# Optimization experiments

Hardware: AMD Instinct MI355X
Metric: run time of the kernel (lower is better)

## Reference

```python
import jax, jax.numpy as jnp
import numpy as np

N = 10000      # nodes
E = 160000     # edges (before self loops)
G = 16         # graphs in batch
H = 4          # attention heads
F = 128        # hidden_dim (per-head out channels)
DIN = 64       # input_dim
NEG_SLOPE = 0.2


def setup_inputs() -> dict:
    key = jax.random.key(0)
    ks = jax.random.split(key, 20)
    x = jax.random.normal(ks[0], (N, DIN), jnp.float32)
    edge_index = jax.random.randint(ks[1], (2, E), 0, N, jnp.int32)
    batch = jnp.sort(jax.random.randint(ks[2], (N,), 0, G, jnp.int32))

    def p(k, shape, scale):
        return (jax.random.normal(k, shape, jnp.float32) * scale).astype(jnp.float32)

    ins = [DIN, H * F, H * F]
    params = {}
    for i in range(3):
        d = ins[i]
        params[f"W{i}"] = p(ks[3 + 4 * i], (d, H * F), (2.0 / (d + F)) ** 0.5)
        params[f"as{i}"] = p(ks[4 + 4 * i], (H, F), 0.1)
        params[f"ad{i}"] = p(ks[5 + 4 * i], (H, F), 0.1)
        bdim = H * F if i < 2 else F
        params[f"b{i}"] = jnp.zeros((bdim,), jnp.float32)
    params["Wr1"] = p(ks[15], (F, F), (2.0 / (2 * F)) ** 0.5)
    params["br1"] = jnp.zeros((F,), jnp.float32)
    params["Wr2"] = p(ks[16], (F, 2 * F), (2.0 / (3 * F)) ** 0.5)
    params["br2"] = jnp.zeros((2 * F,), jnp.float32)
    return {"x": x, "edge_index": edge_index, "batch": batch, **params}


def gat_layer(x, src, dst, W, a_s, a_d, b, concat):
    """PyG-style GATConv (eval mode, self loops already in src/dst)."""
    n = x.shape[0]
    h = (x @ W).reshape(n, H, F)                      # [N,H,F]
    e = jax.nn.leaky_relu(((h * a_s).sum(-1))[src] + ((h * a_d).sum(-1))[dst], NEG_SLOPE)  # [E,H]
    m = jax.ops.segment_max(e, dst, num_segments=n)   # segment softmax over dst
    w = jnp.exp(e - m[dst])
    denom = jax.ops.segment_sum(w, dst, num_segments=n)
    alpha = w / denom[dst]                            # [E,H]
    out = jax.ops.segment_sum(alpha[:, :, None] * h[src], dst, num_segments=n)  # [N,H,F]
    out = out.reshape(n, H * F) if concat else out.mean(axis=1)
    return out + b


def reference(x, edge_index, batch, W0, as0, ad0, b0, W1, as1, ad1, b1,
              W2, as2, ad2, b2, Wr1, br1, Wr2, br2):
    n = x.shape[0]
    loops = jnp.arange(n, dtype=edge_index.dtype)     # add_self_loops (PyG default)
    src = jnp.concatenate([edge_index[0], loops])
    dst = jnp.concatenate([edge_index[1], loops])
    h = jax.nn.relu(gat_layer(x, src, dst, W0, as0, ad0, b0, True))
    h = jax.nn.relu(gat_layer(h, src, dst, W1, as1, ad1, b1, True))
    h = gat_layer(h, src, dst, W2, as2, ad2, b2, False)   # [N,F]
    # global mean pool over graphs
    sums = jax.ops.segment_sum(h, batch, num_segments=G)
    cnt = jax.ops.segment_sum(jnp.ones((n, 1), h.dtype), batch, num_segments=G)
    g = sums / jnp.maximum(cnt, 1.0)                   # [G,F]
    z = jax.nn.relu(g @ Wr1 + br1)
    return z @ Wr2 + br2                               # [G,256]
```

## Files before the change

kernel.cpp:

```cpp
#include <hip/hip_runtime.h>
#include <hip/hip_bf16.h>
#include <math.h>

constexpr int NN  = 10000;
constexpr int NE  = 160000;
constexpr int GG  = 16;
constexpr int HH  = 4;
constexpr int FF  = 128;
constexpr int HF  = 512;
constexpr int DS  = 64;

typedef __attribute__((ext_vector_type(8))) short bf16x8;
typedef __attribute__((ext_vector_type(4))) float f32x4;

__device__ inline short f2bf(float v) {
    __hip_bfloat16 h = __float2bfloat16(v);
    return *reinterpret_cast<short*>(&h);
}
__device__ inline float bf2f(short s) {
    __hip_bfloat16 h = *reinterpret_cast<__hip_bfloat16*>(&s);
    return __bfloat162float(h);
}

__global__ __launch_bounds__(256) void zero_kernel(int* __restrict__ degs,
                                                   float* __restrict__ sums) {
    int i = blockIdx.x * 256 + threadIdx.x;
    if (i < NN) degs[i] = 0;
    if (i < GG * FF) sums[i] = 0.f;
}

__global__ __launch_bounds__(256) void prep_scatter(const float* __restrict__ x,
                                                    short* __restrict__ xb,
                                                    const float* __restrict__ W0,
                                                    const float* __restrict__ W1,
                                                    const float* __restrict__ W2,
                                                    short* __restrict__ T0,
                                                    short* __restrict__ T1,
                                                    short* __restrict__ T2,
                                                    const int* __restrict__ ei,
                                                    int* __restrict__ degs,
                                                    int* __restrict__ adj) {
    int z = blockIdx.z;
    int tid = threadIdx.x;
    int bid = blockIdx.y * 16 + blockIdx.x;
    if (z == 3) {
        const float4* x4 = (const float4*)x;
        for (int i = bid * 256 + tid; i < NN * 16; i += 256 * 256) {
            float4 v = x4[i];
            short4 o;
            o.x = f2bf(v.x); o.y = f2bf(v.y); o.z = f2bf(v.z); o.w = f2bf(v.w);
            *(short4*)&xb[i * 4] = o;
        }
        return;
    }
    if (z == 4) {
        for (int e = bid * 256 + tid; e < NE; e += 256 * 256) {
            int dst = ei[NE + e];
            int pos = atomicAdd(&degs[dst], 1);
            if (pos < DS) adj[dst * DS + pos] = ei[e];
        }
        return;
    }
    const float* W = (z == 0) ? W0 : (z == 1) ? W1 : W2;
    short* T = (z == 0) ? T0 : (z == 1) ? T1 : T2;
    int K = (z == 0) ? 64 : HF;
    int bn = blockIdx.x * 32, bk = blockIdx.y * 32;
    if (bk >= K) return;
    __shared__ float tile[32][33];
    int tx = tid & 31, ty = tid >> 5;
    for (int r = ty; r < 32; r += 8) {
        int k = bk + r, n = bn + tx;
        tile[r][tx] = W[(size_t)k * HF + n];
    }
    __syncthreads();
    for (int r = ty; r < 32; r += 8) {
        int n = bn + r, k = bk + tx;
        T[(size_t)n * K + k] = f2bf(tile[tx][r]);
    }
}

__global__ __launch_bounds__(256) void gemm_attn(const short* __restrict__ A,
                                                 const short* __restrict__ B,
                                                 short* __restrict__ Cb,
                                                 float* __restrict__ es,
                                                 float* __restrict__ ed,
                                                 const float* __restrict__ a_s,
                                                 const float* __restrict__ a_d,
                                                 int M, int K) {
    constexpr int BM = 64, BK = 32, LDT = BK + 8;
    __shared__ short As[BM][LDT];
    __shared__ short Bh[FF][LDT];
    __shared__ float s_red[4][BM][2];
    int tid = threadIdx.x;
    int wave = tid >> 6, lane = tid & 63;
    int fr = lane & 15, fq = lane >> 4;
    int bm = blockIdx.x * BM;
    int head = blockIdx.y;
    int bn = head * FF;
    int arow = tid >> 2, acol = (tid & 3) * 8;
    int brow = tid >> 1, bcol = (tid & 1) * 16;
    f32x4 acc[4][2] = {};
    for (int k0 = 0; k0 < K; k0 += BK) {
        {
            int row = bm + arow;
            bf16x8 va = {};
            if (row < M) va = *(const bf16x8*)&A[(size_t)row * K + k0 + acol];
            *(bf16x8*)&As[arow][acol] = va;
            const short* bsh = &B[(size_t)(bn + brow) * K + k0 + bcol];
            *(bf16x8*)&Bh[brow][bcol]     = *(const bf16x8*)bsh;
            *(bf16x8*)&Bh[brow][bcol + 8] = *(const bf16x8*)(bsh + 8);
        }
        __syncthreads();
        bf16x8 af[4], bh[2];
#pragma unroll
        for (int m = 0; m < 4; m++)
            af[m] = *(const bf16x8*)&As[m * 16 + fr][fq * 8];
#pragma unroll
        for (int n = 0; n < 2; n++)
            bh[n] = *(const bf16x8*)&Bh[wave * 32 + n * 16 + fr][fq * 8];
#pragma unroll
        for (int m = 0; m < 4; m++)
#pragma unroll
            for (int n = 0; n < 2; n++)
                acc[m][n] = __builtin_amdgcn_mfma_f32_16x16x32_bf16(af[m], bh[n], acc[m][n], 0, 0, 0);
        __syncthreads();
    }
    float asv[2], adv[2];
#pragma unroll
    for (int n = 0; n < 2; n++) {
        int c = wave * 32 + n * 16 + fr;
        asv[n] = a_s[head * FF + c];
        adv[n] = a_d[head * FF + c];
    }
#pragma unroll
    for (int m = 0; m < 4; m++) {
#pragma unroll
        for (int j = 0; j < 4; j++) {
            float ps = 0.f, pd = 0.f;
#pragma unroll
            for (int n = 0; n < 2; n++) {
                float v = acc[m][n][j];
                ps += v * asv[n];
                pd += v * adv[n];
            }
#pragma unroll
            for (int o = 1; o < 16; o <<= 1) {
                ps += __shfl_xor(ps, o);
                pd += __shfl_xor(pd, o);
            }
            int rloc = m * 16 + fq * 4 + j;
            if (fr == 0) { s_red[wave][rloc][0] = ps; s_red[wave][rloc][1] = pd; }
            int row = bm + rloc;
            if (row < M) {
#pragma unroll
                for (int n = 0; n < 2; n++)
                    Cb[(size_t)row * HF + bn + wave * 32 + n * 16 + fr] = f2bf(acc[m][n][j]);
            }
        }
    }
    __syncthreads();
    if (tid < BM) {
        int row = bm + tid;
        if (row < M) {
            es[row * 4 + head] = s_red[0][tid][0] + s_red[1][tid][0] +
                                 s_red[2][tid][0] + s_red[3][tid][0];
            ed[row * 4 + head] = s_red[0][tid][1] + s_red[1][tid][1] +
                                 s_red[2][tid][1] + s_red[3][tid][1];
        }
    }
}

template <int MODE>
__global__ __launch_bounds__(256) void gat_aggregate(const short* __restrict__ h,
                                                     const float* __restrict__ es,
                                                     const float* __restrict__ ed,
                                                     const int* __restrict__ degs,
                                                     const int* __restrict__ adj,
                                                     const float* __restrict__ bias,
                                                     float* __restrict__ outf,
                                                     short* __restrict__ outb) {
    constexpr int CAP = DS;
    __shared__ int s_src[4][CAP];
    __shared__ float s_wt[4][4][CAP];
    int tid = threadIdx.x, w = tid >> 6, lane = tid & 63;
    int n = blockIdx.x * 4 + w;
    int deg = min(degs[n], CAP - 1);
    int tot = deg + 1;
    if (lane < tot)
        s_src[w][lane] = (lane < deg) ? adj[n * DS + lane] : n;
    float4 edv = *(const float4*)&ed[n * 4];
    float mx0 = -1e30f, mx1 = -1e30f, mx2 = -1e30f, mx3 = -1e30f;
    if (lane < tot) {
        int s = s_src[w][lane];
        float4 e4 = *(const float4*)&es[s * 4];
        float e0 = e4.x + edv.x; e0 = (e0 >= 0.f) ? e0 : 0.2f * e0;
        float e1 = e4.y + edv.y; e1 = (e1 >= 0.f) ? e1 : 0.2f * e1;
        float e2 = e4.z + edv.z; e2 = (e2 >= 0.f) ? e2 : 0.2f * e2;
        float e3 = e4.w + edv.w; e3 = (e3 >= 0.f) ? e3 : 0.2f * e3;
        s_wt[w][0][lane] = e0; s_wt[w][1][lane] = e1;
        s_wt[w][2][lane] = e2; s_wt[w][3][lane] = e3;
        mx0 = e0; mx1 = e1; mx2 = e2; mx3 = e3;
    }
#pragma unroll
    for (int o = 1; o < 64; o <<= 1) {
        mx0 = fmaxf(mx0, __shfl_xor(mx0, o));
        mx1 = fmaxf(mx1, __shfl_xor(mx1, o));
        mx2 = fmaxf(mx2, __shfl_xor(mx2, o));
        mx3 = fmaxf(mx3, __shfl_xor(mx3, o));
    }
    float s0 = 0.f, s1 = 0.f, s2 = 0.f, s3 = 0.f;
    if (lane < tot) {
        float v0 = __expf(s_wt[w][0][lane] - mx0); s_wt[w][0][lane] = v0; s0 = v0;
        float v1 = __expf(s_wt[w][1][lane] - mx1); s_wt[w][1][lane] = v1; s1 = v1;
        float v2 = __expf(s_wt[w][2][lane] - mx2); s_wt[w][2][lane] = v2; s2 = v2;
        float v3 = __expf(s_wt[w][3][lane] - mx3); s_wt[w][3][lane] = v3; s3 = v3;
    }
#pragma unroll
    for (int o = 1; o < 64; o <<= 1) {
        s0 += __shfl_xor(s0, o); s1 += __shfl_xor(s1, o);
        s2 += __shfl_xor(s2, o); s3 += __shfl_xor(s3, o);
    }
    __syncthreads();
    int head = lane >> 4;
    float rd = 1.f / ((head == 0) ? s0 : (head == 1) ? s1 : (head == 2) ? s2 : s3);
    float acc[8] = {};
    const short* hbase = h + lane * 8;
    for (int i = 0; i < tot; i++) {
        int s = s_src[w][i];
        float wt = s_wt[w][head][i];
        bf16x8 hv = *(const bf16x8*)&hbase[(size_t)s * HF];
#pragma unroll
        for (int k = 0; k < 8; k++) acc[k] += wt * bf2f(hv[k]);
    }
#pragma unroll
    for (int k = 0; k < 8; k++) acc[k] *= rd;
    if (MODE == 0) {
        int c = lane * 8;
        float4 b0 = *(const float4*)&bias[c];
        float4 b1 = *(const float4*)&bias[c + 4];
        bf16x8 o;
        o[0] = f2bf(fmaxf(acc[0] + b0.x, 0.f));
        o[1] = f2bf(fmaxf(acc[1] + b0.y, 0.f));
        o[2] = f2bf(fmaxf(acc[2] + b0.z, 0.f));
        o[3] = f2bf(fmaxf(acc[3] + b0.w, 0.f));
        o[4] = f2bf(fmaxf(acc[4] + b1.x, 0.f));
        o[5] = f2bf(fmaxf(acc[5] + b1.y, 0.f));
        o[6] = f2bf(fmaxf(acc[6] + b1.z, 0.f));
        o[7] = f2bf(fmaxf(acc[7] + b1.w, 0.f));
        *(bf16x8*)&outb[(size_t)n * HF + c] = o;
    } else {
#pragma unroll
        for (int k = 0; k < 8; k++) {
            acc[k] += __shfl_xor(acc[k], 16);
            acc[k] += __shfl_xor(acc[k], 32);
        }
        if (lane < 16) {
            int c = lane * 8;
#pragma unroll
            for (int k = 0; k < 8; k++)
                outf[(size_t)n * FF + c + k] = 0.25f * acc[k] + bias[c + k];
        }
    }
}

__global__ __launch_bounds__(128) void pool_kernel(const float* __restrict__ h2,
                                                   const int* __restrict__ batch,
                                                   float* __restrict__ sums) {
    int f = threadIdx.x;
    int start = blockIdx.x * 64;
    float acc = 0.f;
    int curg = -1;
    for (int i = 0; i < 64; i++) {
        int node = start + i;
        if (node >= NN) break;
        int g = batch[node];
        if (g != curg) {
            if (curg >= 0) atomicAdd(&sums[curg * FF + f], acc);
            acc = 0.f;
            curg = g;
        }
        acc += h2[(size_t)node * FF + f];
    }
    if (curg >= 0) atomicAdd(&sums[curg * FF + f], acc);
}

__global__ __launch_bounds__(256) void mlp_kernel(const float* __restrict__ sums,
                                                  const int* __restrict__ batch,
                                                  const float* __restrict__ Wr1,
                                                  const float* __restrict__ br1,
                                                  const float* __restrict__ Wr2,
                                                  const float* __restrict__ br2,
                                                  float* __restrict__ out) {
    int g = blockIdx.x, t = threadIdx.x;
    __shared__ float gv[128];
    __shared__ float z[128];
    __shared__ float cinv;
    if (t == 0) {
        auto lb = [&](int key) {
            int lo = 0, hi = NN;
            while (lo < hi) { int mid = (lo + hi) >> 1; if (batch[mid] < key) lo = mid + 1; else hi = mid; }
            return lo;
        };
        int cnt = lb(g + 1) - lb(g);
        cinv = 1.0f / fmaxf((float)cnt, 1.0f);
    }
    __syncthreads();
    if (t < 128) gv[t] = sums[g * FF + t] * cinv;
    __syncthreads();
    if (t < 128) {
        float a = br1[t];
        for (int k = 0; k < 128; k++) a += gv[k] * Wr1[k * 128 + t];
        z[t] = fmaxf(a, 0.f);
    }
    __syncthreads();
    {
        float a = br2[t];
        for (int k = 0; k < 128; k++) a += z[k] * Wr2[k * 256 + t];
        out[g * 256 + t] = a;
    }
}

extern "C" void kernel_launch(void* const* d_in, const int* in_sizes, int n_in,
                              void* d_out, int out_size, void* d_ws, size_t ws_size,
                              hipStream_t stream) {
    const float* x    = (const float*)d_in[0];
    const int*   ei   = (const int*)d_in[1];
    const int*   batch= (const int*)d_in[2];
    const float* W0   = (const float*)d_in[3];
    const float* as0  = (const float*)d_in[4];
    const float* ad0  = (const float*)d_in[5];
    const float* b0   = (const float*)d_in[6];
    const float* W1   = (const float*)d_in[7];
    const float* as1  = (const float*)d_in[8];
    const float* ad1  = (const float*)d_in[9];
    const float* b1   = (const float*)d_in[10];
    const float* W2   = (const float*)d_in[11];
    const float* as2  = (const float*)d_in[12];
    const float* ad2  = (const float*)d_in[13];
    const float* b2   = (const float*)d_in[14];
    const float* Wr1  = (const float*)d_in[15];
    const float* br1  = (const float*)d_in[16];
    const float* Wr2  = (const float*)d_in[17];
    const float* br2  = (const float*)d_in[18];
    float* out = (float*)d_out;

    char* p = (char*)d_ws;
    auto alloc = [&](size_t bytes) {
        char* r = p;
        p += (bytes + 255) / 256 * 256;
        return r;
    };
    short* hA      = (short*)alloc((size_t)NN * HF * 2);
    short* hB      = (short*)alloc((size_t)NN * HF * 2);
    float* h2      = (float*)alloc((size_t)NN * FF * 4);
    short* xb      = (short*)alloc((size_t)NN * 64 * 2);
    short* T0      = (short*)alloc((size_t)HF * 64 * 2);
    short* T1      = (short*)alloc((size_t)HF * HF * 2);
    short* T2      = (short*)alloc((size_t)HF * HF * 2);
    float* es      = (float*)alloc((size_t)NN * HH * 4);
    float* ed      = (float*)alloc((size_t)NN * HH * 4);
    int*   degs    = (int*)alloc((size_t)NN * 4);
    int*   adj     = (int*)alloc((size_t)NN * DS * 4);
    float* sums    = (float*)alloc((size_t)GG * FF * 4);

    zero_kernel<<<(NN + 255) / 256, 256, 0, stream>>>(degs, sums);

    prep_scatter<<<dim3(16, 16, 5), 256, 0, stream>>>(x, xb, W0, W1, W2, T0, T1, T2,
                                                      ei, degs, adj);

    dim3 ggemm((NN + 63) / 64, HH);

    gemm_attn<<<ggemm, 256, 0, stream>>>(xb, T0, hA, es, ed, as0, ad0, NN, 64);
    gat_aggregate<0><<<NN / 4, 256, 0, stream>>>(hA, es, ed, degs, adj, b0, nullptr, hB);

    gemm_attn<<<ggemm, 256, 0, stream>>>(hB, T1, hA, es, ed, as1, ad1, NN, HF);
    gat_aggregate<0><<<NN / 4, 256, 0, stream>>>(hA, es, ed, degs, adj, b1, nullptr, hB);

    gemm_attn<<<ggemm, 256, 0, stream>>>(hB, T2, hA, es, ed, as2, ad2, NN, HF);
    gat_aggregate<1><<<NN / 4, 256, 0, stream>>>(hA, es, ed, degs, adj, b2, h2, nullptr);

    pool_kernel<<<(NN + 63) / 64, 128, 0, stream>>>(h2, batch, sums);
    mlp_kernel<<<GG, 256, 0, stream>>>(sums, batch, Wr1, br1, Wr2, br2, out);
}
```

Measured before the change: 191.7 us.

## Double GEMM K-tile, remap blocks for XCD locality, unroll aggregate gather loop

The attention GEMM now stages a K-tile of 64 instead of 32, which halves the number of barrier-separated iterations and issues twice as many MFMAs per sync. The 2D grid becomes a 1D grid whose block index is remapped so consecutive logical tiles (the four heads of the same row block) land on the same XCD and can share the A tile in L2. The gather loop in the aggregate kernel is also unrolled by 4 to raise memory-level parallelism. Costs are more LDS per block and a hardcoded remap formula (79/78 slots per XCD) that assumes exactly 626 blocks, so it is tied to this problem size.

```diff
diff --git a/kernel.cpp b/kernel.cpp
--- a/kernel.cpp
+++ b/kernel.cpp
@@ -87,42 +87,54 @@
                                                  const float* __restrict__ a_s,
                                                  const float* __restrict__ a_d,
                                                  int M, int K) {
-    constexpr int BM = 64, BK = 32, LDT = BK + 8;
+    constexpr int BM = 64, BK = 64, LDT = BK + 8;
     __shared__ short As[BM][LDT];
     __shared__ short Bh[FF][LDT];
     __shared__ float s_red[4][BM][2];
     int tid = threadIdx.x;
     int wave = tid >> 6, lane = tid & 63;
     int fr = lane & 15, fq = lane >> 4;
-    int bm = blockIdx.x * BM;
-    int head = blockIdx.y;
+    int b = blockIdx.x;
+    int xcd = b & 7, slot = b >> 3;
+    int l = (xcd < 4 ? xcd * 79 : 316 + (xcd - 4) * 78) + slot;
+    int bm = (l >> 2) * BM;
+    int head = l & 3;
     int bn = head * FF;
-    int arow = tid >> 2, acol = (tid & 3) * 8;
-    int brow = tid >> 1, bcol = (tid & 1) * 16;
+    int srow = tid >> 3, scol = (tid & 7) * 8;
     f32x4 acc[4][2] = {};
     for (int k0 = 0; k0 < K; k0 += BK) {
-        {
-            int row = bm + arow;
+#pragma unroll
+        for (int p = 0; p < 2; p++) {
+            int r = srow + 32 * p;
+            int row = bm + r;
             bf16x8 va = {};
-            if (row < M) va = *(const bf16x8*)&A[(size_t)row * K + k0 + acol];
-            *(bf16x8*)&As[arow][acol] = va;
-            const short* bsh = &B[(size_t)(bn + brow) * K + k0 + bcol];
-            *(bf16x8*)&Bh[brow][bcol]     = *(const bf16x8*)bsh;
-            *(bf16x8*)&Bh[brow][bcol + 8] = *(const bf16x8*)(bsh + 8);
+            if (row < M) va = *(const bf16x8*)&A[(size_t)row * K + k0 + scol];
+            *(bf16x8*)&As[r][scol] = va;
+        }
+#pragma unroll
+        for (int p = 0; p < 4; p++) {
+            int r = srow + 32 * p;
+            *(bf16x8*)&Bh[r][scol] = *(const bf16x8*)&B[(size_t)(bn + r) * K + k0 + scol];
         }
         __syncthreads();
-        bf16x8 af[4], bh[2];
-#pragma unroll
-        for (int m = 0; m < 4; m++)
-            af[m] = *(const bf16x8*)&As[m * 16 + fr][fq * 8];
-#pragma unroll
-        for (int n = 0; n < 2; n++)
-            bh[n] = *(const bf16x8*)&Bh[wave * 32 + n * 16 + fr][fq * 8];
-#pragma unroll
-        for (int m = 0; m < 4; m++)
+        bf16x8 af[2][4], bh[2][2];
+#pragma unroll
+        for (int kk = 0; kk < 2; kk++) {
+#pragma unroll
+            for (int m = 0; m < 4; m++)
+                af[kk][m] = *(const bf16x8*)&As[m * 16 + fr][kk * 32 + fq * 8];
 #pragma unroll
             for (int n = 0; n < 2; n++)
-                acc[m][n] = __builtin_amdgcn_mfma_f32_16x16x32_bf16(af[m], bh[n], acc[m][n], 0, 0, 0);
+                bh[kk][n] = *(const bf16x8*)&Bh[wave * 32 + n * 16 + fr][kk * 32 + fq * 8];
+        }
+#pragma unroll
+        for (int kk = 0; kk < 2; kk++)
+#pragma unroll
+            for (int m = 0; m < 4; m++)
+#pragma unroll
+                for (int n = 0; n < 2; n++)
+                    acc[m][n] = __builtin_amdgcn_mfma_f32_16x16x32_bf16(af[kk][m], bh[kk][n],
+                                                                        acc[m][n], 0, 0, 0);
         __syncthreads();
     }
     float asv[2], adv[2];
@@ -225,6 +237,7 @@
     float rd = 1.f / ((head == 0) ? s0 : (head == 1) ? s1 : (head == 2) ? s2 : s3);
     float acc[8] = {};
     const short* hbase = h + lane * 8;
+#pragma unroll 4
     for (int i = 0; i < tot; i++) {
         int s = s_src[w][i];
         float wt = s_wt[w][head][i];
@@ -368,15 +381,15 @@
     prep_scatter<<<dim3(16, 16, 5), 256, 0, stream>>>(x, xb, W0, W1, W2, T0, T1, T2,
                                                       ei, degs, adj);
 
-    dim3 ggemm((NN + 63) / 64, HH);
-
-    gemm_attn<<<ggemm, 256, 0, stream>>>(xb, T0, hA, es, ed, as0, ad0, NN, 64);
+    int ngemm = ((NN + 63) / 64) * HH;
+
+    gemm_attn<<<ngemm, 256, 0, stream>>>(xb, T0, hA, es, ed, as0, ad0, NN, 64);
     gat_aggregate<0><<<NN / 4, 256, 0, stream>>>(hA, es, ed, degs, adj, b0, nullptr, hB);
 
-    gemm_attn<<<ggemm, 256, 0, stream>>>(hB, T1, hA, es, ed, as1, ad1, NN, HF);
+    gemm_attn<<<ngemm, 256, 0, stream>>>(hB, T1, hA, es, ed, as1, ad1, NN, HF);
     gat_aggregate<0><<<NN / 4, 256, 0, stream>>>(hA, es, ed, degs, adj, b1, nullptr, hB);
 
-    gemm_attn<<<ggemm, 256, 0, stream>>>(hB, T2, hA, es, ed, as2, ad2, NN, HF);
+    gemm_attn<<<ngemm, 256, 0, stream>>>(hB, T2, hA, es, ed, as2, ad2, NN, HF);
     gat_aggregate<1><<<NN / 4, 256, 0, stream>>>(hA, es, ed, degs, adj, b2, h2, nullptr);
 
     pool_kernel<<<(NN + 63) / 64, 128, 0, stream>>>(h2, batch, sums);
```

After: 195.8 us. 2.1% more time.
